# Kernel optimization log

Hardware: AMD Instinct MI355X
Metric: run time of the kernel (lower is better)

Reference implementation:

```python
import jax, jax.numpy as jnp
import numpy as np

N = 8192       # node_num
F_IN = 256     # src_feature
F_OUT = 128    # out_feature
NEG_SLOPE = 0.2  # standard GAT leakyrelu slope
MASK_VAL = -1e12


def setup_inputs() -> dict:
    key = jax.random.key(0)
    k1, k2, k3, k4, k5, k6 = jax.random.split(key, 6)
    x = jax.random.normal(k1, (N, F_IN), dtype=jnp.float32)
    adj = jax.random.randint(k2, (N, N), 0, 2, dtype=jnp.int32)  # 0/1 adjacency mask
    # xavier-uniform-like scales
    W = jax.random.normal(k3, (F_IN, F_OUT), dtype=jnp.float32) * np.float32(1.0 / np.sqrt(F_IN))
    a1 = jax.random.normal(k4, (F_OUT,), dtype=jnp.float32) * np.float32(0.1)  # att[:F_OUT]
    a2 = jax.random.normal(k5, (F_OUT,), dtype=jnp.float32) * np.float32(0.1)  # att[F_OUT:]
    bias = jax.random.normal(k6, (F_OUT,), dtype=jnp.float32) * np.float32(0.1)
    return {"x": x, "adj": adj, "W": W, "a1": a1, "a2": a2, "bias": bias}


def reference(x, adj, W, a1, a2, bias):
    # h = x @ W1  (src_h == dst_h for int src_dst_feature)
    h = x @ W  # [N, F_OUT]
    # e[i,j] = leakyrelu(att^T [h_i || h_j]) decomposed as (h@a1)_i + (h@a2)_j
    s_src = h @ a1  # [N]
    s_dst = h @ a2  # [N]
    e = jax.nn.leaky_relu(s_src[:, None] + s_dst[None, :], NEG_SLOPE)  # [N, N]
    masked = jnp.where(adj > 0, e, jnp.float32(MASK_VAL))
    attention = jax.nn.softmax(masked, axis=1)  # [N, N]
    # dropout in eval mode = identity; aggregate neighbor features
    out = attention @ h + bias  # [N, F_OUT]
    return out
```

## Files before the change

### kernel.cpp

```cpp
#include <hip/hip_runtime.h>
#include <cstdint>
#include <cstddef>

#define NN 8192
#define FIN 256
#define FOUT 128
#define SLOPE 0.2f
#define SHIFT 8.0f

typedef float f32x4 __attribute__((ext_vector_type(4)));
typedef __bf16 bf16x8 __attribute__((ext_vector_type(8)));
typedef int i32x4 __attribute__((ext_vector_type(4)));
typedef unsigned int u32x4 __attribute__((ext_vector_type(4)));

__device__ __forceinline__ unsigned short f2bf(float f) {
  return __builtin_bit_cast(unsigned short, (__bf16)f);
}

__device__ __forceinline__ void async_cp16(void* lds, const void* g) {
  __builtin_amdgcn_global_load_lds(
      (const __attribute__((address_space(1))) void*)g,
      (__attribute__((address_space(3))) void*)lds, 16, 0, 0);
}

__global__ __launch_bounds__(256, 4) void k_hw(const float* __restrict__ x,
                                               const float* __restrict__ W,
                                               const float* __restrict__ a1,
                                               const float* __restrict__ a2,
                                               unsigned short* __restrict__ ht,
                                               float* __restrict__ Etab,
                                               unsigned short* __restrict__ FbfF,
                                               unsigned short* __restrict__ FbfF2) {
  __shared__ float xs[8][256];
  __shared__ unsigned short tile[128][8];
  const int tid = threadIdx.x;
  const int rowbase = blockIdx.x * 8;

  #pragma unroll
  for (int it = 0; it < 2; ++it) {
    int fi = it * 1024 + tid * 4;
    int r = fi >> 8, k = fi & 255;
    *(f32x4*)&xs[r][k] = *(const f32x4*)(x + (size_t)(rowbase + r) * FIN + k);
  }
  __syncthreads();

  const int r = tid >> 5;
  const int cg = tid & 31;
  f32x4 acc = {0.f, 0.f, 0.f, 0.f};

  #pragma unroll 8
  for (int k = 0; k < FIN; ++k) {
    f32x4 wv = *(const f32x4*)(W + k * FOUT + cg * 4);
    float xv = xs[r][k];
    acc[0] += xv * wv[0];
    acc[1] += xv * wv[1];
    acc[2] += xv * wv[2];
    acc[3] += xv * wv[3];
  }

  #pragma unroll
  for (int c = 0; c < 4; ++c) tile[cg * 4 + c][r] = f2bf(acc[c]);

  f32x4 av1 = *(const f32x4*)(a1 + cg * 4);
  f32x4 av2 = *(const f32x4*)(a2 + cg * 4);
  float s1 = acc[0] * av1[0] + acc[1] * av1[1] + acc[2] * av1[2] + acc[3] * av1[3];
  float s2 = acc[0] * av2[0] + acc[1] * av2[1] + acc[2] * av2[2] + acc[3] * av2[3];
  #pragma unroll
  for (int off = 16; off > 0; off >>= 1) {
    s1 += __shfl_xor(s1, off, 64);
    s2 += __shfl_xor(s2, off, 64);
  }
  if (cg == 0) {
    const int row = rowbase + r;
    float c0 = s1 + SHIFT;
    float c = fmaxf(c0, SLOPE * c0);
    Etab[(size_t)row * 2]     = __expf(s1 - c);
    Etab[(size_t)row * 2 + 1] = __expf(SLOPE * s1 - c);
    FbfF[row]  = f2bf(__expf(s2));
    FbfF2[row] = f2bf(__expf(SLOPE * s2));
  }
  __syncthreads();

  if (tid < 128) {
    u32x4 v = *(const u32x4*)&tile[tid][0];
    *(u32x4*)(ht + (size_t)tid * NN + rowbase) = v;
  }
}

__global__ __launch_bounds__(256) void k_zero(float* __restrict__ outacc,
                                              float* __restrict__ dws) {
  const int i = blockIdx.x * 256 + threadIdx.x;
  f32x4 z = {0.f, 0.f, 0.f, 0.f};
  ((f32x4*)outacc)[i] = z;
  if (i < NN / 4) ((f32x4*)dws)[i] = z;
}

__global__ __launch_bounds__(256, 4) void k_gat(const int* __restrict__ adj,
                                                const unsigned short* __restrict__ ht,
                                                const float* __restrict__ Etab,
                                                const unsigned short* __restrict__ FbfF,
                                                const unsigned short* __restrict__ FbfF2,
                                                float* __restrict__ outacc,
                                                float* __restrict__ dws) {
  __shared__ unsigned short sH[2][128 * 64];
  __shared__ unsigned short sF[2][128];

  const int tid = threadIdx.x;
  const int wave = tid >> 6;
  const int lane = tid & 63;
  const int quad = lane >> 4;
  const int m = lane & 15;
  const int rowbase = (int)(blockIdx.x >> 1) * 16;
  const int colbase = (int)(blockIdx.x & 1) * (NN / 2);
  const int row = rowbase + m;

  bf16x8 pm, pinv, pones;
  #pragma unroll
  for (int jj = 0; jj < 8; ++jj) {
    pm[jj] = (__bf16)(float)m;
    pinv[jj] = (__bf16)0.03125f;
    pones[jj] = (__bf16)1.0f;
  }
  f32x4 z = {0.f, 0.f, 0.f, 0.f};
  f32x4 rp = __builtin_amdgcn_mfma_f32_16x16x32_bf16(pm, pinv, z, 0, 0, 0);
  f32x4 cp = __builtin_amdgcn_mfma_f32_16x16x32_bf16(pinv, pm, z, 0, 0, 0);
  int rowmap[4], colmap[4];
  #pragma unroll
  for (int r = 0; r < 4; ++r) {
    rowmap[r] = ((int)(rp[r] + 0.5f)) & 15;
    colmap[r] = ((int)(cp[r] + 0.5f)) & 15;
  }

  const float E  = Etab[(size_t)row * 2];
  const float E2 = Etab[(size_t)row * 2 + 1];
  const int t0 = wave * 2, t1 = wave * 2 + 1;

  f32x4 acc0 = z, acc1 = z, den = z;

  const unsigned short* srcH[4];
  #pragma unroll
  for (int il = 0; il < 4; ++il) {
    const int i = wave * 4 + il;
    const int f = i * 8 + (lane >> 3);
    const int g = (lane & 7) ^ (lane >> 3);
    srcH[il] = ht + (size_t)f * NN + colbase + g * 8;
  }
  const unsigned short* srcF = nullptr;
  if (wave == 1) {
    srcF = (lane < 8) ? (FbfF + colbase + lane * 8)
                      : (FbfF2 + colbase + (lane - 8) * 8);
  }

  auto stage = [&](int b) {
    #pragma unroll
    for (int il = 0; il < 4; ++il) {
      async_cp16(&sH[b][(wave * 4 + il) * 512], srcH[il]);
      srcH[il] += 64;
    }
    if (wave == 1 && lane < 16) {
      async_cp16(&sF[b][0], srcF);
      srcF += 64;
    }
  };

  const int* arow = adj + (size_t)row * NN + colbase + quad * 8;
  auto load_adj = [&](i32x4* d, int c) {
    const int* p = arow + c * 64;
    d[0] = *(const i32x4*)(p);
    d[1] = *(const i32x4*)(p + 4);
    d[2] = *(const i32x4*)(p + 32);
    d[3] = *(const i32x4*)(p + 36);
  };

  auto compute = [&](int cs, const i32x4* av) {
    #pragma unroll
    for (int k32 = 0; k32 < 2; ++k32) {
      const int jl = k32 * 32 + quad * 8;
      u32x4 Fq = *(const u32x4*)&sF[cs][jl];
      u32x4 Gq = *(const u32x4*)&sF[cs][64 + jl];
      const i32x4 A0 = av[k32 * 2];
      const i32x4 A1 = av[k32 * 2 + 1];

      bf16x8 af;
      #pragma unroll
      for (int p = 0; p < 4; ++p) {
        const unsigned fp = Fq[p], gp = Gq[p];
        const float Flo = __builtin_bit_cast(float, fp << 16);
        const float Fhi = __builtin_bit_cast(float, fp & 0xffff0000u);
        const float Glo = __builtin_bit_cast(float, gp << 16);
        const float Ghi = __builtin_bit_cast(float, gp & 0xffff0000u);
        const float wlo = fmaxf(E * Flo, E2 * Glo);
        const float whi = fmaxf(E * Fhi, E2 * Ghi);
        const int avlo = (p < 2) ? A0[p * 2] : A1[p * 2 - 4];
        const int avhi = (p < 2) ? A0[p * 2 + 1] : A1[p * 2 - 3];
        af[p * 2]     = avlo ? (__bf16)wlo : (__bf16)0.0f;
        af[p * 2 + 1] = avhi ? (__bf16)whi : (__bf16)0.0f;
      }

      const int s0 = (k32 * 4 + quad) ^ (m & 7);
      bf16x8 b0 = __builtin_bit_cast(bf16x8,
          *(const u32x4*)&sH[cs][(t0 * 16 + m) * 64 + s0 * 8]);
      bf16x8 b1 = __builtin_bit_cast(bf16x8,
          *(const u32x4*)&sH[cs][(t1 * 16 + m) * 64 + s0 * 8]);

      acc0 = __builtin_amdgcn_mfma_f32_16x16x32_bf16(af, b0, acc0, 0, 0, 0);
      acc1 = __builtin_amdgcn_mfma_f32_16x16x32_bf16(af, b1, acc1, 0, 0, 0);
      den  = __builtin_amdgcn_mfma_f32_16x16x32_bf16(af, pones, den, 0, 0, 0);
    }
  };

  i32x4 aA[4], aB[4];
  load_adj(aA, 0);
  stage(0);

  #pragma unroll 1
  for (int c = 0; c < 64; c += 2) {
    __syncthreads();
    stage(1);
    load_adj(aB, c + 1);
    compute(0, aA);
    __syncthreads();
    if (c + 2 < 64) {
      stage(0);
      load_adj(aA, c + 2);
    }
    compute(1, aB);
  }

  #pragma unroll
  for (int r = 0; r < 4; ++r) {
    const int orow = rowbase + rowmap[r];
    const int c0 = t0 * 16 + colmap[r];
    const int c1 = t1 * 16 + colmap[r];
    atomicAdd(&outacc[(size_t)orow * FOUT + c0], acc0[r]);
    atomicAdd(&outacc[(size_t)orow * FOUT + c1], acc1[r]);
  }
  if (wave == 0 && m == 0) {
    #pragma unroll
    for (int r = 0; r < 4; ++r) {
      atomicAdd(&dws[rowbase + rowmap[r]], den[r]);
    }
  }
}

__global__ __launch_bounds__(256) void k_fin(const float* __restrict__ dws,
                                             const float* __restrict__ bias,
                                             float* __restrict__ out) {
  const int idx = (blockIdx.x * 256 + threadIdx.x) * 4;
  const int rowi = idx >> 7;
  const int f = idx & 127;
  const float inv = 1.0f / dws[rowi];
  f32x4 v = *(f32x4*)(out + idx);
  f32x4 b = *(const f32x4*)(bias + f);
  v[0] = v[0] * inv + b[0];
  v[1] = v[1] * inv + b[1];
  v[2] = v[2] * inv + b[2];
  v[3] = v[3] * inv + b[3];
  *(f32x4*)(out + idx) = v;
}

extern "C" void kernel_launch(void* const* d_in, const int* in_sizes, int n_in,
                              void* d_out, int out_size, void* d_ws, size_t ws_size,
                              hipStream_t stream) {
  const float* x    = (const float*)d_in[0];
  const int*   adj  = (const int*)d_in[1];
  const float* W    = (const float*)d_in[2];
  const float* a1   = (const float*)d_in[3];
  const float* a2   = (const float*)d_in[4];
  const float* bias = (const float*)d_in[5];
  float* out = (float*)d_out;

  char* ws = (char*)d_ws;
  unsigned short* ht = (unsigned short*)ws;
  float* Etab = (float*)(ws + (size_t)2 * 1024 * 1024);
  unsigned short* FbfF =
      (unsigned short*)(ws + (size_t)2 * 1024 * 1024 + 64 * 1024);
  unsigned short* FbfF2 = FbfF + NN;
  float* dws = (float*)(ws + (size_t)2 * 1024 * 1024 + 96 * 1024);

  k_zero<<<(NN * FOUT / 4) / 256, 256, 0, stream>>>(out, dws);
  k_hw<<<NN / 8, 256, 0, stream>>>(x, W, a1, a2, ht, Etab, FbfF, FbfF2);
  k_gat<<<(NN / 16) * 2, 256, 0, stream>>>(adj, ht, Etab, FbfF, FbfF2, out, dws);
  k_fin<<<(NN * FOUT / 4) / 256, 256, 0, stream>>>(dws, bias, out);
}
```

Before: 509.3 us.

## Stream adjacency tiles through LDS via async copies and fold zeroing into k_hw

The adjacency rows are now staged into a swizzled, double-buffered LDS tile with global_load_lds async copies issued by waves 2-3, replacing the per-thread direct global register loads. The F/G exponent tables, which were previously staged in LDS, are now loaded straight into registers. The separate zeroing kernel is removed, and k_hw clears the output and denominator buffers instead. The goal is to overlap the dominant 256MB adjacency stream with compute and to save one kernel launch, at the cost of extra LDS use and possible bank conflicts.

```diff
diff --git a/kernel.cpp b/kernel.cpp
--- a/kernel.cpp
+++ b/kernel.cpp
@@ -30,11 +30,19 @@
                                                unsigned short* __restrict__ ht,
                                                float* __restrict__ Etab,
                                                unsigned short* __restrict__ FbfF,
-                                               unsigned short* __restrict__ FbfF2) {
+                                               unsigned short* __restrict__ FbfF2,
+                                               float* __restrict__ outacc,
+                                               float* __restrict__ dws) {
   __shared__ float xs[8][256];
   __shared__ unsigned short tile[128][8];
   const int tid = threadIdx.x;
   const int rowbase = blockIdx.x * 8;
+
+  {
+    f32x4 z = {0.f, 0.f, 0.f, 0.f};
+    *(f32x4*)(outacc + (size_t)blockIdx.x * 1024 + tid * 4) = z;
+    if (tid < 2) *(f32x4*)(dws + blockIdx.x * 8 + tid * 4) = z;
+  }
 
   #pragma unroll
   for (int it = 0; it < 2; ++it) {
@@ -87,14 +95,6 @@
   }
 }
 
-__global__ __launch_bounds__(256) void k_zero(float* __restrict__ outacc,
-                                              float* __restrict__ dws) {
-  const int i = blockIdx.x * 256 + threadIdx.x;
-  f32x4 z = {0.f, 0.f, 0.f, 0.f};
-  ((f32x4*)outacc)[i] = z;
-  if (i < NN / 4) ((f32x4*)dws)[i] = z;
-}
-
 __global__ __launch_bounds__(256, 4) void k_gat(const int* __restrict__ adj,
                                                 const unsigned short* __restrict__ ht,
                                                 const float* __restrict__ Etab,
@@ -102,8 +102,8 @@
                                                 const unsigned short* __restrict__ FbfF2,
                                                 float* __restrict__ outacc,
                                                 float* __restrict__ dws) {
+  __shared__ int sA[2][16 * 64];
   __shared__ unsigned short sH[2][128 * 64];
-  __shared__ unsigned short sF[2][128];
 
   const int tid = threadIdx.x;
   const int wave = tid >> 6;
@@ -145,10 +145,17 @@
     const int g = (lane & 7) ^ (lane >> 3);
     srcH[il] = ht + (size_t)f * NN + colbase + g * 8;
   }
-  const unsigned short* srcF = nullptr;
-  if (wave == 1) {
-    srcF = (lane < 8) ? (FbfF + colbase + lane * 8)
-                      : (FbfF2 + colbase + (lane - 8) * 8);
+  const int* srcA[2] = {nullptr, nullptr};
+  int slotA[2] = {0, 0};
+  if (wave >= 2) {
+    #pragma unroll
+    for (int q2 = 0; q2 < 2; ++q2) {
+      const int il = (wave - 2) * 2 + q2;
+      const int r = il * 4 + (lane >> 4);
+      const int g = (lane & 15) ^ r;
+      slotA[q2] = il;
+      srcA[q2] = adj + (size_t)(rowbase + r) * NN + colbase + g * 4;
+    }
   }
 
   auto stage = [&](int b) {
@@ -157,29 +164,35 @@
       async_cp16(&sH[b][(wave * 4 + il) * 512], srcH[il]);
       srcH[il] += 64;
     }
-    if (wave == 1 && lane < 16) {
-      async_cp16(&sF[b][0], srcF);
-      srcF += 64;
+    if (wave >= 2) {
+      #pragma unroll
+      for (int q2 = 0; q2 < 2; ++q2) {
+        async_cp16(&sA[b][slotA[q2] * 256], srcA[q2]);
+        srcA[q2] += 64;
+      }
     }
   };
 
-  const int* arow = adj + (size_t)row * NN + colbase + quad * 8;
-  auto load_adj = [&](i32x4* d, int c) {
-    const int* p = arow + c * 64;
-    d[0] = *(const i32x4*)(p);
-    d[1] = *(const i32x4*)(p + 4);
-    d[2] = *(const i32x4*)(p + 32);
-    d[3] = *(const i32x4*)(p + 36);
+  const unsigned short* fbase = FbfF  + colbase + quad * 8;
+  const unsigned short* gbase = FbfF2 + colbase + quad * 8;
+  struct Fregs { u32x4 F0, F1, G0, G1; };
+  auto load_f = [&](Fregs& d, int c) {
+    const unsigned short* p = fbase + c * 64;
+    const unsigned short* q = gbase + c * 64;
+    d.F0 = *(const u32x4*)(p);
+    d.F1 = *(const u32x4*)(p + 32);
+    d.G0 = *(const u32x4*)(q);
+    d.G1 = *(const u32x4*)(q + 32);
   };
 
-  auto compute = [&](int cs, const i32x4* av) {
+  auto compute = [&](int cs, const Fregs& fr) {
     #pragma unroll
     for (int k32 = 0; k32 < 2; ++k32) {
-      const int jl = k32 * 32 + quad * 8;
-      u32x4 Fq = *(const u32x4*)&sF[cs][jl];
-      u32x4 Gq = *(const u32x4*)&sF[cs][64 + jl];
-      const i32x4 A0 = av[k32 * 2];
-      const i32x4 A1 = av[k32 * 2 + 1];
+      const int g0 = k32 * 8 + quad * 2;
+      i32x4 A0 = *(const i32x4*)&sA[cs][m * 64 + ((g0) ^ m) * 4];
+      i32x4 A1 = *(const i32x4*)&sA[cs][m * 64 + ((g0 + 1) ^ m) * 4];
+      const u32x4 Fq = k32 ? fr.F1 : fr.F0;
+      const u32x4 Gq = k32 ? fr.G1 : fr.G0;
 
       bf16x8 af;
       #pragma unroll
@@ -209,22 +222,22 @@
     }
   };
 
-  i32x4 aA[4], aB[4];
-  load_adj(aA, 0);
+  Fregs fA, fB;
+  load_f(fA, 0);
   stage(0);
 
   #pragma unroll 1
   for (int c = 0; c < 64; c += 2) {
     __syncthreads();
     stage(1);
-    load_adj(aB, c + 1);
-    compute(0, aA);
+    load_f(fB, c + 1);
+    compute(0, fA);
     __syncthreads();
     if (c + 2 < 64) {
       stage(0);
-      load_adj(aA, c + 2);
-    }
-    compute(1, aB);
+      load_f(fA, c + 2);
+    }
+    compute(1, fB);
   }
 
   #pragma unroll
@@ -278,8 +291,7 @@
   unsigned short* FbfF2 = FbfF + NN;
   float* dws = (float*)(ws + (size_t)2 * 1024 * 1024 + 96 * 1024);
 
-  k_zero<<<(NN * FOUT / 4) / 256, 256, 0, stream>>>(out, dws);
-  k_hw<<<NN / 8, 256, 0, stream>>>(x, W, a1, a2, ht, Etab, FbfF, FbfF2);
+  k_hw<<<NN / 8, 256, 0, stream>>>(x, W, a1, a2, ht, Etab, FbfF, FbfF2, out, dws);
   k_gat<<<(NN / 16) * 2, 256, 0, stream>>>(adj, ht, Etab, FbfF, FbfF2, out, dws);
   k_fin<<<(NN * FOUT / 4) / 256, 256, 0, stream>>>(dws, bias, out);
 }
```

Measured after the change: 464.8 us. -8.7%, faster.

## Pack adjacency to bitmasks and retile GAT kernel to 128-row blocks

Applied to the files above, without the earlier changes.

A new k_pack kernel turns the int32 adjacency into per-row bitmasks using wave ballots. k_gat now reads these packed bits through LDS and uses 512-thread blocks covering 128 rows × 1024 columns. Each wave computes all 8 feature tiles, so every staged H tile is shared by eight row groups instead of one. Output zeroing moves into k_hw, which removes the separate k_zero launch. The adjacency still has to be read once in full by the pack kernel, and the larger per-wave accumulators raise register pressure.

```diff
diff --git a/kernel.cpp b/kernel.cpp
--- a/kernel.cpp
+++ b/kernel.cpp
@@ -21,6 +21,38 @@
   __builtin_amdgcn_global_load_lds(
       (const __attribute__((address_space(1))) void*)g,
       (__attribute__((address_space(3))) void*)lds, 16, 0, 0);
+}
+__device__ __forceinline__ void async_cp4(void* lds, const void* g) {
+  __builtin_amdgcn_global_load_lds(
+      (const __attribute__((address_space(1))) void*)g,
+      (__attribute__((address_space(3))) void*)lds, 4, 0, 0);
+}
+
+__global__ __launch_bounds__(256) void k_pack(const int* __restrict__ adj,
+                                              unsigned int* __restrict__ adjp) {
+  const int gw = (blockIdx.x * 256 + threadIdx.x) >> 6;
+  const int lane = threadIdx.x & 63;
+  #pragma unroll 1
+  for (int qt = gw; qt < 8192 * 32; qt += 8192) {
+    const int row = qt >> 5;
+    const int j256 = qt & 31;
+    const int* p = adj + (size_t)row * NN + j256 * 256 + lane;
+    const int a0 = p[0];
+    const int a1 = p[64];
+    const int a2 = p[128];
+    const int a3 = p[192];
+    const unsigned long long m0 = __ballot(a0 != 0);
+    const unsigned long long m1 = __ballot(a1 != 0);
+    const unsigned long long m2 = __ballot(a2 != 0);
+    const unsigned long long m3 = __ballot(a3 != 0);
+    if (lane == 0) {
+      unsigned int* d = adjp + (size_t)row * 256 + j256 * 8;
+      u32x4 v0 = {(unsigned)m0, (unsigned)(m0 >> 32), (unsigned)m1, (unsigned)(m1 >> 32)};
+      u32x4 v1 = {(unsigned)m2, (unsigned)(m2 >> 32), (unsigned)m3, (unsigned)(m3 >> 32)};
+      *(u32x4*)(d) = v0;
+      *(u32x4*)(d + 4) = v1;
+    }
+  }
 }
 
 __global__ __launch_bounds__(256, 4) void k_hw(const float* __restrict__ x,
@@ -30,11 +62,19 @@
                                                unsigned short* __restrict__ ht,
                                                float* __restrict__ Etab,
                                                unsigned short* __restrict__ FbfF,
-                                               unsigned short* __restrict__ FbfF2) {
+                                               unsigned short* __restrict__ FbfF2,
+                                               float* __restrict__ outacc,
+                                               float* __restrict__ dws) {
   __shared__ float xs[8][256];
   __shared__ unsigned short tile[128][8];
   const int tid = threadIdx.x;
   const int rowbase = blockIdx.x * 8;
+
+  {
+    f32x4 z = {0.f, 0.f, 0.f, 0.f};
+    *(f32x4*)(outacc + (size_t)blockIdx.x * 1024 + tid * 4) = z;
+    if (tid < 2) *(f32x4*)(dws + blockIdx.x * 8 + tid * 4) = z;
+  }
 
   #pragma unroll
   for (int it = 0; it < 2; ++it) {
@@ -87,15 +127,7 @@
   }
 }
 
-__global__ __launch_bounds__(256) void k_zero(float* __restrict__ outacc,
-                                              float* __restrict__ dws) {
-  const int i = blockIdx.x * 256 + threadIdx.x;
-  f32x4 z = {0.f, 0.f, 0.f, 0.f};
-  ((f32x4*)outacc)[i] = z;
-  if (i < NN / 4) ((f32x4*)dws)[i] = z;
-}
-
-__global__ __launch_bounds__(256, 4) void k_gat(const int* __restrict__ adj,
+__global__ __launch_bounds__(512, 4) void k_gat(const unsigned int* __restrict__ adjp,
                                                 const unsigned short* __restrict__ ht,
                                                 const float* __restrict__ Etab,
                                                 const unsigned short* __restrict__ FbfF,
@@ -103,6 +135,7 @@
                                                 float* __restrict__ outacc,
                                                 float* __restrict__ dws) {
   __shared__ unsigned short sH[2][128 * 64];
+  __shared__ unsigned int sAp[2][2][128];
   __shared__ unsigned short sF[2][128];
 
   const int tid = threadIdx.x;
@@ -110,9 +143,9 @@
   const int lane = tid & 63;
   const int quad = lane >> 4;
   const int m = lane & 15;
-  const int rowbase = (int)(blockIdx.x >> 1) * 16;
-  const int colbase = (int)(blockIdx.x & 1) * (NN / 2);
-  const int row = rowbase + m;
+  const int rowbase = (int)(blockIdx.x >> 3) * 128;
+  const int colbase = (int)(blockIdx.x & 7) * 1024;
+  const int row = rowbase + wave * 16 + m;
 
   bf16x8 pm, pinv, pones;
   #pragma unroll
@@ -133,17 +166,24 @@
 
   const float E  = Etab[(size_t)row * 2];
   const float E2 = Etab[(size_t)row * 2 + 1];
-  const int t0 = wave * 2, t1 = wave * 2 + 1;
-
-  f32x4 acc0 = z, acc1 = z, den = z;
-
-  const unsigned short* srcH[4];
-  #pragma unroll
-  for (int il = 0; il < 4; ++il) {
-    const int i = wave * 4 + il;
+
+  f32x4 acc[8];
+  #pragma unroll
+  for (int t = 0; t < 8; ++t) acc[t] = z;
+  f32x4 den = z;
+
+  const unsigned short* srcH[2];
+  #pragma unroll
+  for (int il = 0; il < 2; ++il) {
+    const int i = wave * 2 + il;
     const int f = i * 8 + (lane >> 3);
     const int g = (lane & 7) ^ (lane >> 3);
     srcH[il] = ht + (size_t)f * NN + colbase + g * 8;
+  }
+  const unsigned int* srcAp = nullptr;
+  if (wave == 2 || wave == 3) {
+    const int lr = (wave - 2) * 64 + lane;
+    srcAp = adjp + (size_t)(rowbase + lr) * (NN / 32) + (colbase >> 5);
   }
   const unsigned short* srcF = nullptr;
   if (wave == 1) {
@@ -151,35 +191,26 @@
                       : (FbfF2 + colbase + (lane - 8) * 8);
   }
 
-  auto stage = [&](int b) {
+  auto stage = [&](int b, int c) {
     #pragma unroll
-    for (int il = 0; il < 4; ++il) {
-      async_cp16(&sH[b][(wave * 4 + il) * 512], srcH[il]);
-      srcH[il] += 64;
-    }
-    if (wave == 1 && lane < 16) {
-      async_cp16(&sF[b][0], srcF);
-      srcF += 64;
+    for (int il = 0; il < 2; ++il)
+      async_cp16(&sH[b][(wave * 2 + il) * 512], srcH[il] + c * 64);
+    if (wave == 1 && lane < 16) async_cp16(&sF[b][0], srcF + c * 64);
+    if (wave == 2 || wave == 3) {
+      #pragma unroll
+      for (int q = 0; q < 2; ++q)
+        async_cp4(&sAp[b][q][(wave - 2) * 64], srcAp + c * 2 + q);
     }
   };
 
-  const int* arow = adj + (size_t)row * NN + colbase + quad * 8;
-  auto load_adj = [&](i32x4* d, int c) {
-    const int* p = arow + c * 64;
-    d[0] = *(const i32x4*)(p);
-    d[1] = *(const i32x4*)(p + 4);
-    d[2] = *(const i32x4*)(p + 32);
-    d[3] = *(const i32x4*)(p + 36);
-  };
-
-  auto compute = [&](int cs, const i32x4* av) {
+  auto compute = [&](int cs) {
     #pragma unroll
     for (int k32 = 0; k32 < 2; ++k32) {
+      const unsigned int word = sAp[cs][k32][wave * 16 + m];
+      const unsigned int byt = (word >> (quad * 8)) & 0xffu;
       const int jl = k32 * 32 + quad * 8;
       u32x4 Fq = *(const u32x4*)&sF[cs][jl];
       u32x4 Gq = *(const u32x4*)&sF[cs][64 + jl];
-      const i32x4 A0 = av[k32 * 2];
-      const i32x4 A1 = av[k32 * 2 + 1];
 
       bf16x8 af;
       #pragma unroll
@@ -191,54 +222,45 @@
         const float Ghi = __builtin_bit_cast(float, gp & 0xffff0000u);
         const float wlo = fmaxf(E * Flo, E2 * Glo);
         const float whi = fmaxf(E * Fhi, E2 * Ghi);
-        const int avlo = (p < 2) ? A0[p * 2] : A1[p * 2 - 4];
-        const int avhi = (p < 2) ? A0[p * 2 + 1] : A1[p * 2 - 3];
-        af[p * 2]     = avlo ? (__bf16)wlo : (__bf16)0.0f;
-        af[p * 2 + 1] = avhi ? (__bf16)whi : (__bf16)0.0f;
+        af[p * 2]     = (byt & (1u << (p * 2)))     ? (__bf16)wlo : (__bf16)0.0f;
+        af[p * 2 + 1] = (byt & (1u << (p * 2 + 1))) ? (__bf16)whi : (__bf16)0.0f;
       }
 
       const int s0 = (k32 * 4 + quad) ^ (m & 7);
-      bf16x8 b0 = __builtin_bit_cast(bf16x8,
-          *(const u32x4*)&sH[cs][(t0 * 16 + m) * 64 + s0 * 8]);
-      bf16x8 b1 = __builtin_bit_cast(bf16x8,
-          *(const u32x4*)&sH[cs][(t1 * 16 + m) * 64 + s0 * 8]);
-
-      acc0 = __builtin_amdgcn_mfma_f32_16x16x32_bf16(af, b0, acc0, 0, 0, 0);
-      acc1 = __builtin_amdgcn_mfma_f32_16x16x32_bf16(af, b1, acc1, 0, 0, 0);
-      den  = __builtin_amdgcn_mfma_f32_16x16x32_bf16(af, pones, den, 0, 0, 0);
+      #pragma unroll
+      for (int t = 0; t < 8; ++t) {
+        bf16x8 bt = __builtin_bit_cast(bf16x8,
+            *(const u32x4*)&sH[cs][(t * 16 + m) * 64 + s0 * 8]);
+        acc[t] = __builtin_amdgcn_mfma_f32_16x16x32_bf16(af, bt, acc[t], 0, 0, 0);
+      }
+      den = __builtin_amdgcn_mfma_f32_16x16x32_bf16(af, pones, den, 0, 0, 0);
     }
   };
 
-  i32x4 aA[4], aB[4];
-  load_adj(aA, 0);
-  stage(0);
+  stage(0, 0);
 
   #pragma unroll 1
-  for (int c = 0; c < 64; c += 2) {
+  for (int c = 0; c < 16; c += 2) {
     __syncthreads();
-    stage(1);
-    load_adj(aB, c + 1);
-    compute(0, aA);
+    stage(1, c + 1);
+    compute(0);
     __syncthreads();
-    if (c + 2 < 64) {
-      stage(0);
-      load_adj(aA, c + 2);
-    }
-    compute(1, aB);
+    if (c + 2 < 16) stage(0, c + 2);
+    compute(1);
   }
 
   #pragma unroll
   for (int r = 0; r < 4; ++r) {
-    const int orow = rowbase + rowmap[r];
-    const int c0 = t0 * 16 + colmap[r];
-    const int c1 = t1 * 16 + colmap[r];
-    atomicAdd(&outacc[(size_t)orow * FOUT + c0], acc0[r]);
-    atomicAdd(&outacc[(size_t)orow * FOUT + c1], acc1[r]);
-  }
-  if (wave == 0 && m == 0) {
+    const int orow = rowbase + wave * 16 + rowmap[r];
+    #pragma unroll
+    for (int t = 0; t < 8; ++t) {
+      atomicAdd(&outacc[(size_t)orow * FOUT + t * 16 + colmap[r]], acc[t][r]);
+    }
+  }
+  if (m == 0) {
     #pragma unroll
     for (int r = 0; r < 4; ++r) {
-      atomicAdd(&dws[rowbase + rowmap[r]], den[r]);
+      atomicAdd(&dws[rowbase + wave * 16 + rowmap[r]], den[r]);
     }
   }
 }
@@ -277,9 +299,11 @@
       (unsigned short*)(ws + (size_t)2 * 1024 * 1024 + 64 * 1024);
   unsigned short* FbfF2 = FbfF + NN;
   float* dws = (float*)(ws + (size_t)2 * 1024 * 1024 + 96 * 1024);
-
-  k_zero<<<(NN * FOUT / 4) / 256, 256, 0, stream>>>(out, dws);
-  k_hw<<<NN / 8, 256, 0, stream>>>(x, W, a1, a2, ht, Etab, FbfF, FbfF2);
-  k_gat<<<(NN / 16) * 2, 256, 0, stream>>>(adj, ht, Etab, FbfF, FbfF2, out, dws);
+  unsigned int* adjp =
+      (unsigned int*)(ws + (size_t)2 * 1024 * 1024 + 128 * 1024);
+
+  k_pack<<<2048, 256, 0, stream>>>(adj, adjp);
+  k_hw<<<NN / 8, 256, 0, stream>>>(x, W, a1, a2, ht, Etab, FbfF, FbfF2, out, dws);
+  k_gat<<<512, 512, 0, stream>>>(adjp, ht, Etab, FbfF, FbfF2, out, dws);
   k_fin<<<(NN * FOUT / 4) / 256, 256, 0, stream>>>(dws, bias, out);
 }
```

Result: faster. 465.0 us (-8.7%).
